# Performance work log

Measured on AMD Instinct MI355X. Metric: run time of the kernel, lower is better.

## Reference

```python
import jax, jax.numpy as jnp
import numpy as np

B, C_IN, C_OUT, P, NN, NA, KS = 1, 32, 64, 1024, 24, 60, 4
RADIUS, SIGMA, EPS = 0.4, 0.08, 1e-5


def setup_inputs() -> dict:
    key = jax.random.key(0)
    k = jax.random.split(key, 6)
    xyz = jax.random.normal(k[0], (B, 3, P), dtype=jnp.float32)
    feats = jax.random.normal(k[1], (B, C_IN, P, NA), dtype=jnp.float32)
    inter_idx = jax.random.randint(k[2], (B, P, NN), 0, P)
    # anchors: NA proper rotation matrices (icosahedral-group stand-in) via QR
    m = jax.random.normal(k[3], (NA, 3, 3), dtype=jnp.float32)
    q, r = jnp.linalg.qr(m)
    q = q * jnp.sign(jnp.diagonal(r, axis1=-2, axis2=-1))[:, None, :]
    det = jnp.linalg.det(q)
    anchors = q.at[:, :, 0].set(q[:, :, 0] * det[:, None])  # det = +1
    # kernel points sampled inside the conv radius
    kernels = (jax.random.uniform(k[4], (KS, 3), dtype=jnp.float32) * 2.0 - 1.0) * (RADIUS * 0.7)
    W = jax.random.normal(k[5], (C_OUT, C_IN * KS), dtype=jnp.float32) * (1.0 / np.sqrt(C_IN * KS))
    return {"xyz": xyz, "feats": feats, "inter_idx": inter_idx,
            "anchors": anchors, "kernels": kernels, "W": W}


def reference(xyz, feats, inter_idx, anchors, kernels, W):
    # neighbor gather of coordinates: [B,3,P,NN]
    gxyz = jax.vmap(lambda x, i: x[:, i])(xyz, inter_idx)
    rel = gxyz - xyz[:, :, :, None]                       # relative coords
    # anchor-rotated kernel points: [NA,KS,3]
    rk = jnp.einsum('aij,kj->aki', anchors, kernels)
    # squared distances without materializing [B,3,NA,KS,P,NN]
    d2 = (jnp.sum(rel * rel, axis=1)[:, None, None]                    # [B,1,1,P,NN]
          + jnp.sum(rk * rk, axis=-1)[None, :, :, None, None]          # [1,NA,KS,1,1]
          - 2.0 * jnp.einsum('bdpn,akd->bakpn', rel, rk))              # [B,NA,KS,P,NN]
    inter_w = jax.nn.relu(1.0 - d2 / SIGMA)                            # linear falloff
    # neighbor gather of features: [B,C,P,NN,NA]
    gfeats = jax.vmap(lambda f, i: f[:, i, :])(feats, inter_idx)
    # kernel-weighted aggregation over neighbors: [B,C,KS,P,NA]
    fk = jnp.einsum('bcpna,bakpn->bckpa', gfeats, inter_w)
    # BasicZPConv GEMM: W [C_OUT, C_IN*KS] over flattened (c,ks)
    out = jnp.einsum('dck,bckpa->bdpa', W.reshape(C_OUT, C_IN, KS), fk)  # [B,C_OUT,P,NA]
    # InstanceNorm2d(affine=False) over (P,NA) per (batch, channel), then ReLU
    mu = jnp.mean(out, axis=(2, 3), keepdims=True)
    var = jnp.var(out, axis=(2, 3), keepdims=True)
    feat = jax.nn.relu((out - mu) * jax.lax.rsqrt(var + EPS))
    return feat
```

## Files before the change

### kernel.cpp

```cpp
#include <hip/hip_runtime.h>

#define CIN  32
#define COUT 64
#define PP   1024
#define NN   24
#define NA   60
#define KS   4
#define PA   (PP*NA)
#define CK   (CIN*KS)
#define FKLD 136
constexpr float SIGMA_INV = 12.5f;
constexpr float EPS = 1e-5f;

typedef __attribute__((ext_vector_type(8))) short short8;
typedef __attribute__((ext_vector_type(4))) float floatx4;

__device__ inline unsigned f2bf1(float f) {
    unsigned u = __float_as_uint(f);
    return (u + 0x7fffu + ((u >> 16) & 1u)) >> 16;
}
__device__ inline unsigned packbf(float lo, float hi) {
    return f2bf1(lo) | (f2bf1(hi) << 16);
}

__global__ __launch_bounds__(256, 4) void k1_fused(
    const float* __restrict__ xyz,
    const float* __restrict__ feats,
    const int*   __restrict__ inter_idx,
    const float* __restrict__ anchors,
    const float* __restrict__ kern,
    const float* __restrict__ W,
    float* __restrict__ out,
    float* __restrict__ psum,
    float* __restrict__ psq)
{
    const int p      = blockIdx.x;
    const int tid    = threadIdx.x;
    const int g      = tid >> 6;
    const int l      = tid & 63;
    const int lane15 = l & 15;
    const int quad   = l >> 4;
    const bool valid = (l < NA);
    const int  a     = valid ? l : (NA - 1);

    __shared__ float4 s_rel[NN];
    __shared__ int    s_idx[NN];
    __shared__ unsigned short s_fk[64 * FKLD];

    if (tid < NN) {
        int j = inter_idx[p * NN + tid];
        s_idx[tid] = j;
        float rx = xyz[j]          - xyz[p];
        float ry = xyz[PP + j]     - xyz[PP + p];
        float rz = xyz[2 * PP + j] - xyz[2 * PP + p];
        s_rel[tid] = make_float4(rx, ry, rz, rx * rx + ry * ry + rz * rz);
    }

    float Cw[KS], Rx[KS], Ry[KS], Rz[KS];
    {
        const float* A = anchors + a * 9;
        float a00 = A[0], a01 = A[1], a02 = A[2];
        float a10 = A[3], a11 = A[4], a12 = A[5];
        float a20 = A[6], a21 = A[7], a22 = A[8];
        #pragma unroll
        for (int k = 0; k < KS; ++k) {
            float kx = kern[k * 3 + 0], ky = kern[k * 3 + 1], kz = kern[k * 3 + 2];
            float r0 = a00 * kx + a01 * ky + a02 * kz;
            float r1 = a10 * kx + a11 * ky + a12 * kz;
            float r2 = a20 * kx + a21 * ky + a22 * kz;
            Cw[k] = 1.0f - SIGMA_INV * (r0 * r0 + r1 * r1 + r2 * r2);
            Rx[k] = 2.0f * SIGMA_INV * r0;
            Ry[k] = 2.0f * SIGMA_INV * r1;
            Rz[k] = 2.0f * SIGMA_INV * r2;
        }
    }
    __syncthreads();

    float acc[8][KS];
    #pragma unroll
    for (int c = 0; c < 8; ++c)
        #pragma unroll
        for (int k = 0; k < KS; ++k) acc[c][k] = 0.0f;

    #pragma unroll 4
    for (int n = 0; n < NN; ++n) {
        float4 rel = s_rel[n];
        int j = s_idx[n];
        const float* fb = feats + (size_t)(g * 8) * PA + (size_t)j * NA + a;
        float f[8];
        #pragma unroll
        for (int c = 0; c < 8; ++c)
            f[c] = fb[(size_t)c * PA];
        float tb = -SIGMA_INV * rel.w;
        float w[KS];
        #pragma unroll
        for (int k = 0; k < KS; ++k) {
            float v = Cw[k] + tb;
            v = fmaf(rel.x, Rx[k], v);
            v = fmaf(rel.y, Ry[k], v);
            v = fmaf(rel.z, Rz[k], v);
            w[k] = v > 0.0f ? v : 0.0f;
        }
        #pragma unroll
        for (int c = 0; c < 8; ++c)
            #pragma unroll
            for (int k = 0; k < KS; ++k)
                acc[c][k] = fmaf(f[c], w[k], acc[c][k]);
    }

    {
        unsigned pk[16];
        #pragma unroll
        for (int c = 0; c < 8; ++c) {
            pk[c * 2 + 0] = valid ? packbf(acc[c][0], acc[c][1]) : 0u;
            pk[c * 2 + 1] = valid ? packbf(acc[c][2], acc[c][3]) : 0u;
        }
        uint4* dst = (uint4*)&s_fk[(size_t)l * FKLD + g * 32];
        dst[0] = make_uint4(pk[0],  pk[1],  pk[2],  pk[3]);
        dst[1] = make_uint4(pk[4],  pk[5],  pk[6],  pk[7]);
        dst[2] = make_uint4(pk[8],  pk[9],  pk[10], pk[11]);
        dst[3] = make_uint4(pk[12], pk[13], pk[14], pk[15]);
    }

    short8 afrag[4];
    {
        const float* wbase = W + (size_t)(g * 16 + lane15) * CK + quad * 8;
        #pragma unroll
        for (int ks = 0; ks < 4; ++ks) {
            float4 w0 = *(const float4*)(wbase + ks * 32);
            float4 w1 = *(const float4*)(wbase + ks * 32 + 4);
            union { short8 s; unsigned u[4]; } pa;
            pa.u[0] = packbf(w0.x, w0.y);
            pa.u[1] = packbf(w0.z, w0.w);
            pa.u[2] = packbf(w1.x, w1.y);
            pa.u[3] = packbf(w1.z, w1.w);
            afrag[ks] = pa.s;
        }
    }

    __syncthreads();

    floatx4 cacc[4];
    #pragma unroll
    for (int t = 0; t < 4; ++t) cacc[t] = (floatx4){0.f, 0.f, 0.f, 0.f};

    #pragma unroll
    for (int ks = 0; ks < 4; ++ks) {
        #pragma unroll
        for (int t = 0; t < 4; ++t) {
            short8 bfrag = *(const short8*)&s_fk[(size_t)(t * 16 + lane15) * FKLD + ks * 32 + quad * 8];
            cacc[t] = __builtin_amdgcn_mfma_f32_16x16x32_bf16(afrag[ks], bfrag, cacc[t], 0, 0, 0);
        }
    }

    const int d0 = g * 16;
    float ssum[4] = {0.f, 0.f, 0.f, 0.f}, ssq[4] = {0.f, 0.f, 0.f, 0.f};
    #pragma unroll
    for (int t = 0; t < 4; ++t) {
        int acol = t * 16 + lane15;
        bool vcol = acol < NA;
        #pragma unroll
        for (int r = 0; r < 4; ++r) {
            float v = cacc[t][r];
            int d = d0 + quad * 4 + r;
            if (vcol) out[(size_t)d * PA + (size_t)p * NA + acol] = v;
            ssum[r] += v;
            ssq[r]  += v * v;
        }
    }
    #pragma unroll
    for (int r = 0; r < 4; ++r) {
        float ss = ssum[r], qq = ssq[r];
        #pragma unroll
        for (int off = 8; off; off >>= 1) {
            ss += __shfl_down(ss, off, 16);
            qq += __shfl_down(qq, off, 16);
        }
        if (lane15 == 0) {
            int d = d0 + quad * 4 + r;
            psum[d * PP + p] = ss;
            psq [d * PP + p] = qq;
        }
    }
}

__global__ __launch_bounds__(256) void k3_norm(
    const float* __restrict__ psum, const float* __restrict__ psq,
    float* __restrict__ out)
{
    const int d   = blockIdx.y;
    const int tid = threadIdx.x;

    float4 ps = ((const float4*)(psum + d * PP))[tid];
    float4 qs = ((const float4*)(psq  + d * PP))[tid];
    float s = ps.x + ps.y + ps.z + ps.w;
    float q = qs.x + qs.y + qs.z + qs.w;
    #pragma unroll
    for (int off = 32; off; off >>= 1) {
        s += __shfl_down(s, off, 64);
        q += __shfl_down(q, off, 64);
    }
    __shared__ float sred[8];
    __shared__ float s_mu, s_rs;
    int w = tid >> 6;
    if ((tid & 63) == 0) { sred[w] = s; sred[4 + w] = q; }
    __syncthreads();
    if (tid == 0) {
        float S = sred[0] + sred[1] + sred[2] + sred[3];
        float Q = sred[4] + sred[5] + sred[6] + sred[7];
        const float inv = 1.0f / (float)PA;
        float mu  = S * inv;
        float var = Q * inv - mu * mu;
        s_mu = mu;
        s_rs = rsqrtf(var + EPS);
    }
    __syncthreads();
    const float mu = s_mu, rs = s_rs;

    size_t base = (size_t)d * PA + (size_t)blockIdx.x * 1024 + tid * 4;
    float4* po = (float4*)(out + base);
    float4 v = *po;
    v.x = fmaxf((v.x - mu) * rs, 0.f);
    v.y = fmaxf((v.y - mu) * rs, 0.f);
    v.z = fmaxf((v.z - mu) * rs, 0.f);
    v.w = fmaxf((v.w - mu) * rs, 0.f);
    *po = v;
}

extern "C" void kernel_launch(void* const* d_in, const int* in_sizes, int n_in,
                              void* d_out, int out_size, void* d_ws, size_t ws_size,
                              hipStream_t stream) {
    const float* xyz     = (const float*)d_in[0];
    const float* feats   = (const float*)d_in[1];
    const int*   idx     = (const int*)d_in[2];
    const float* anchors = (const float*)d_in[3];
    const float* kern    = (const float*)d_in[4];
    const float* W       = (const float*)d_in[5];
    float* out = (float*)d_out;

    float* ws   = (float*)d_ws;
    float* psum = ws;
    float* psq  = psum + COUT * PP;

    hipLaunchKernelGGL(k1_fused, dim3(PP), dim3(256), 0, stream,
                       xyz, feats, idx, anchors, kern, W, out, psum, psq);
    hipLaunchKernelGGL(k3_norm, dim3(PA / 1024, COUT), dim3(256), 0, stream,
                       psum, psq, out);
}
```

Baseline: 102.2 us.

## Split each point's anchors across two blocks to reduce idle lanes and registers

Each point is now handled by two blocks, each covering 30 anchors. Lanes are re-mapped so that 32 lanes cover anchors and 2 lanes per wave split channels, which removes the 4 idle lanes of 64 and halves the per-thread accumulators. Launch bounds are raised to 8 blocks per SM, the MFMA tile count drops to 2, and the partial-sum buffers double, with the norm kernel reading both halves. In exchange, neighbor indices, relative coordinates and W fragments are loaded twice per point, and the feature loads become half-wave runs of 30 floats.

```diff
diff --git a/kernel.cpp b/kernel.cpp
--- a/kernel.cpp
+++ b/kernel.cpp
@@ -9,6 +9,7 @@
 #define PA   (PP*NA)
 #define CK   (CIN*KS)
 #define FKLD 136
+#define NB   (PP*2)
 constexpr float SIGMA_INV = 12.5f;
 constexpr float EPS = 1e-5f;
 
@@ -23,7 +24,7 @@
     return f2bf1(lo) | (f2bf1(hi) << 16);
 }
 
-__global__ __launch_bounds__(256, 4) void k1_fused(
+__global__ __launch_bounds__(256, 8) void k1_fused(
     const float* __restrict__ xyz,
     const float* __restrict__ feats,
     const int*   __restrict__ inter_idx,
@@ -34,18 +35,23 @@
     float* __restrict__ psum,
     float* __restrict__ psq)
 {
-    const int p      = blockIdx.x;
+    const int half   = blockIdx.x & 1;
+    const int p      = blockIdx.x >> 1;
     const int tid    = threadIdx.x;
     const int g      = tid >> 6;
     const int l      = tid & 63;
     const int lane15 = l & 15;
     const int quad   = l >> 4;
-    const bool valid = (l < NA);
-    const int  a     = valid ? l : (NA - 1);
+    const int aloc   = l & 31;
+    const int csub   = l >> 5;
+    const bool valid = (aloc < 30);
+    const int  acl   = valid ? aloc : 29;
+    const int  a     = half * 30 + acl;
+    const int  cbase = (g * 2 + csub) * 4;
 
     __shared__ float4 s_rel[NN];
     __shared__ int    s_idx[NN];
-    __shared__ unsigned short s_fk[64 * FKLD];
+    __shared__ unsigned short s_fk[32 * FKLD];
 
     if (tid < NN) {
         int j = inter_idx[p * NN + tid];
@@ -76,9 +82,9 @@
     }
     __syncthreads();
 
-    float acc[8][KS];
-    #pragma unroll
-    for (int c = 0; c < 8; ++c)
+    float acc[4][KS];
+    #pragma unroll
+    for (int c = 0; c < 4; ++c)
         #pragma unroll
         for (int k = 0; k < KS; ++k) acc[c][k] = 0.0f;
 
@@ -86,10 +92,10 @@
     for (int n = 0; n < NN; ++n) {
         float4 rel = s_rel[n];
         int j = s_idx[n];
-        const float* fb = feats + (size_t)(g * 8) * PA + (size_t)j * NA + a;
-        float f[8];
-        #pragma unroll
-        for (int c = 0; c < 8; ++c)
+        const float* fb = feats + (size_t)cbase * PA + (size_t)j * NA + half * 30 + acl;
+        float f[4];
+        #pragma unroll
+        for (int c = 0; c < 4; ++c)
             f[c] = fb[(size_t)c * PA];
         float tb = -SIGMA_INV * rel.w;
         float w[KS];
@@ -102,24 +108,22 @@
             w[k] = v > 0.0f ? v : 0.0f;
         }
         #pragma unroll
-        for (int c = 0; c < 8; ++c)
+        for (int c = 0; c < 4; ++c)
             #pragma unroll
             for (int k = 0; k < KS; ++k)
                 acc[c][k] = fmaf(f[c], w[k], acc[c][k]);
     }
 
     {
-        unsigned pk[16];
-        #pragma unroll
-        for (int c = 0; c < 8; ++c) {
+        unsigned pk[8];
+        #pragma unroll
+        for (int c = 0; c < 4; ++c) {
             pk[c * 2 + 0] = valid ? packbf(acc[c][0], acc[c][1]) : 0u;
             pk[c * 2 + 1] = valid ? packbf(acc[c][2], acc[c][3]) : 0u;
         }
-        uint4* dst = (uint4*)&s_fk[(size_t)l * FKLD + g * 32];
-        dst[0] = make_uint4(pk[0],  pk[1],  pk[2],  pk[3]);
-        dst[1] = make_uint4(pk[4],  pk[5],  pk[6],  pk[7]);
-        dst[2] = make_uint4(pk[8],  pk[9],  pk[10], pk[11]);
-        dst[3] = make_uint4(pk[12], pk[13], pk[14], pk[15]);
+        uint4* dst = (uint4*)&s_fk[(size_t)aloc * FKLD + cbase * 4];
+        dst[0] = make_uint4(pk[0], pk[1], pk[2], pk[3]);
+        dst[1] = make_uint4(pk[4], pk[5], pk[6], pk[7]);
     }
 
     short8 afrag[4];
@@ -140,14 +144,14 @@
 
     __syncthreads();
 
-    floatx4 cacc[4];
-    #pragma unroll
-    for (int t = 0; t < 4; ++t) cacc[t] = (floatx4){0.f, 0.f, 0.f, 0.f};
+    floatx4 cacc[2];
+    #pragma unroll
+    for (int t = 0; t < 2; ++t) cacc[t] = (floatx4){0.f, 0.f, 0.f, 0.f};
 
     #pragma unroll
     for (int ks = 0; ks < 4; ++ks) {
         #pragma unroll
-        for (int t = 0; t < 4; ++t) {
+        for (int t = 0; t < 2; ++t) {
             short8 bfrag = *(const short8*)&s_fk[(size_t)(t * 16 + lane15) * FKLD + ks * 32 + quad * 8];
             cacc[t] = __builtin_amdgcn_mfma_f32_16x16x32_bf16(afrag[ks], bfrag, cacc[t], 0, 0, 0);
         }
@@ -156,14 +160,14 @@
     const int d0 = g * 16;
     float ssum[4] = {0.f, 0.f, 0.f, 0.f}, ssq[4] = {0.f, 0.f, 0.f, 0.f};
     #pragma unroll
-    for (int t = 0; t < 4; ++t) {
-        int acol = t * 16 + lane15;
-        bool vcol = acol < NA;
+    for (int t = 0; t < 2; ++t) {
+        int am = t * 16 + lane15;
+        bool vcol = am < 30;
         #pragma unroll
         for (int r = 0; r < 4; ++r) {
             float v = cacc[t][r];
             int d = d0 + quad * 4 + r;
-            if (vcol) out[(size_t)d * PA + (size_t)p * NA + acol] = v;
+            if (vcol) out[(size_t)d * PA + (size_t)p * NA + half * 30 + am] = v;
             ssum[r] += v;
             ssq[r]  += v * v;
         }
@@ -178,8 +182,8 @@
         }
         if (lane15 == 0) {
             int d = d0 + quad * 4 + r;
-            psum[d * PP + p] = ss;
-            psq [d * PP + p] = qq;
+            psum[d * NB + blockIdx.x] = ss;
+            psq [d * NB + blockIdx.x] = qq;
         }
     }
 }
@@ -191,10 +195,12 @@
     const int d   = blockIdx.y;
     const int tid = threadIdx.x;
 
-    float4 ps = ((const float4*)(psum + d * PP))[tid];
-    float4 qs = ((const float4*)(psq  + d * PP))[tid];
-    float s = ps.x + ps.y + ps.z + ps.w;
-    float q = qs.x + qs.y + qs.z + qs.w;
+    float4 p0 = ((const float4*)(psum + (size_t)d * NB))[tid];
+    float4 p1 = ((const float4*)(psum + (size_t)d * NB))[tid + 256];
+    float4 q0 = ((const float4*)(psq  + (size_t)d * NB))[tid];
+    float4 q1 = ((const float4*)(psq  + (size_t)d * NB))[tid + 256];
+    float s = p0.x + p0.y + p0.z + p0.w + p1.x + p1.y + p1.z + p1.w;
+    float q = q0.x + q0.y + q0.z + q0.w + q1.x + q1.y + q1.z + q1.w;
     #pragma unroll
     for (int off = 32; off; off >>= 1) {
         s += __shfl_down(s, off, 64);
@@ -240,9 +246,9 @@
 
     float* ws   = (float*)d_ws;
     float* psum = ws;
-    float* psq  = psum + COUT * PP;
-
-    hipLaunchKernelGGL(k1_fused, dim3(PP), dim3(256), 0, stream,
+    float* psq  = psum + COUT * NB;
+
+    hipLaunchKernelGGL(k1_fused, dim3(NB), dim3(256), 0, stream,
                        xyz, feats, idx, anchors, kern, W, out, psum, psq);
     hipLaunchKernelGGL(k3_norm, dim3(PA / 1024, COUT), dim3(256), 0, stream,
                        psum, psq, out);
```

Result: slower. 120.4 us (+17.8%).
